# Optimization experiments

Measured on AMD Instinct MI355X. Metric: run time of the kernel, lower is better.

Reference implementation:

```python
import jax, jax.numpy as jnp
import numpy as np

B, IH, IW = 16, 32, 32
N = IH * IW
HEADS, DIM_HEAD = 8, 64
INNER = HEADS * DIM_HEAD  # 512
INP, OUP = 512, 512
SCALE = DIM_HEAD ** -0.5


def _relative_index():
    # replicate torch.meshgrid (ij) -> coords [2, N]
    yy, xx = np.meshgrid(np.arange(IH), np.arange(IW), indexing='ij')
    coords = np.stack([yy.reshape(-1), xx.reshape(-1)])  # [2, N]
    rel = coords[:, :, None] - coords[:, None, :]        # [2, N, N]
    rel[0] += IH - 1
    rel[1] += IW - 1
    rel[0] *= 2 * IW - 1
    return jnp.asarray(rel.sum(0).reshape(-1), dtype=jnp.int32)  # [N*N]


def setup_inputs() -> dict:
    key = jax.random.key(0)
    k1, k2, k3, k4, k5 = jax.random.split(key, 5)
    x = jax.random.normal(k1, (B, N, INP), dtype=jnp.float32)
    W_qkv = jax.random.normal(k2, (INP, 3 * INNER), dtype=jnp.float32) * (INP ** -0.5)
    # table is initialized to zeros in the module; use small randn so bias path is exercised
    rel_table = jax.random.normal(k3, ((2 * IH - 1) * (2 * IW - 1), HEADS), dtype=jnp.float32) * 0.02
    W_out = jax.random.normal(k4, (INNER, OUP), dtype=jnp.float32) * (INNER ** -0.5)
    b_out = jax.random.normal(k5, (OUP,), dtype=jnp.float32) * 0.02
    return {
        'x': x,
        'W_qkv': W_qkv,
        'rel_table': rel_table,
        'W_out': W_out,
        'b_out': b_out,
        'rel_index': _relative_index(),
    }


def reference(x, W_qkv, rel_table, W_out, b_out, rel_index):
    b, n, _ = x.shape
    qkv = x @ W_qkv                                            # [b, n, 3*inner]
    q, k, v = jnp.split(qkv, 3, axis=-1)
    def to_heads(t):
        return t.reshape(b, n, HEADS, DIM_HEAD).transpose(0, 2, 1, 3)  # [b, h, n, d]
    q, k, v = to_heads(q), to_heads(k), to_heads(v)
    dots = jnp.einsum('bhnd,bhmd->bhnm', q, k) * SCALE         # [b, h, n, n]
    bias = rel_table[rel_index].reshape(n, n, HEADS).transpose(2, 0, 1)[None]  # [1, h, n, n]
    attn = jax.nn.softmax(dots + bias, axis=-1)
    out = jnp.einsum('bhnm,bhmd->bhnd', attn, v)               # [b, h, n, d]
    out = out.transpose(0, 2, 1, 3).reshape(b, n, INNER)       # [b, n, inner]
    return out @ W_out + b_out
```

## Files before the change

kernel.cpp:

```cpp
#include <hip/hip_runtime.h>
#include <math.h>

#define BATCH 16
#define NTOK 1024
#define HEADS 8
#define DHEAD 64
#define INNER 512
#define QKV_COLS 1536
#define SCALE_L2E 0.1803368801111244f
#define LOG2E 1.4426950408889634f

#if __has_builtin(__builtin_amdgcn_exp2f)
#define EXP2F(x) __builtin_amdgcn_exp2f(x)
#else
#define EXP2F(x) __expf((x) * 0.6931471805599453f)
#endif

typedef _Float16 f16x8 __attribute__((ext_vector_type(8)));
typedef _Float16 f16x4 __attribute__((ext_vector_type(4)));
typedef float f32x4 __attribute__((ext_vector_type(4)));

#define MFMA32(a, b, c) __builtin_amdgcn_mfma_f32_16x16x32_f16(a, b, c, 0, 0, 0)

__device__ __forceinline__ void glds16(const void* g, void* l) {
    __builtin_amdgcn_global_load_lds(
        (const __attribute__((address_space(1))) unsigned int*)g,
        (__attribute__((address_space(3))) unsigned int*)l, 16, 0, 0);
}

#define XV (BATCH * NTOK * INNER / 4)
#define WQ (INNER * QKV_COLS)
#define WO (INNER * INNER)

__global__ __launch_bounds__(256)
void convert_inputs(const float* __restrict__ x, const float* __restrict__ Wq,
                    const float* __restrict__ Wo, _Float16* __restrict__ x_h,
                    _Float16* __restrict__ Wq_t, _Float16* __restrict__ Wo_t) {
    int idx = blockIdx.x * 256 + threadIdx.x;
    if (idx < XV) {
        float4 v = ((const float4*)x)[idx];
        f16x4 h;
        h[0] = (_Float16)v.x; h[1] = (_Float16)v.y;
        h[2] = (_Float16)v.z; h[3] = (_Float16)v.w;
        *(f16x4*)(x_h + (size_t)idx * 4) = h;
    } else if (idx < XV + WQ) {
        int i = idx - XV;
        int n = i >> 9, k = i & 511;
        Wq_t[i] = (_Float16)Wq[k * QKV_COLS + n];
    } else if (idx < XV + WQ + WO) {
        int i = idx - XV - WQ;
        int n = i >> 9, k = i & 511;
        Wo_t[i] = (_Float16)Wo[k * INNER + n];
    }
}

__global__ __launch_bounds__(256, 2)
void gemm_qkv(const _Float16* __restrict__ A, const _Float16* __restrict__ Bt,
              _Float16* __restrict__ qkv, _Float16* __restrict__ vtg,
              int M, int N, int K) {
    __shared__ _Float16 As[3][128 * 32];
    __shared__ _Float16 Bs[3][256 * 32];

    const int t    = threadIdx.x;
    const int l    = t & 63;
    const int w    = t >> 6;
    const int wm   = w >> 1;
    const int wn   = w & 1;
    const int quad = l >> 4;
    const int lrow = l & 15;

    const int nwg = gridDim.x * gridDim.y;
    int bid = blockIdx.x + gridDim.x * blockIdx.y;
    bid = (bid & 7) * (nwg >> 3) + (bid >> 3);
    const size_t row0 = (size_t)(bid / gridDim.x) * 128;
    const size_t col0 = (size_t)(bid % gridDim.x) * 256;

    const int srow = t >> 2;
    const int sch  = t & 3;

    f32x4 acc[4][8] = {};
    const int NSTEP = K >> 5;

    auto stage = [&](int kk, int bufi) {
#pragma unroll
        for (int p = 0; p < 2; ++p) {
            const int r  = p * 64 + srow;
            const int gc = (sch ^ ((r >> 1) & 3)) * 8;
            glds16(A + (row0 + r) * K + kk * 32 + gc,
                   (char*)As[bufi] + p * 4096 + t * 16);
        }
#pragma unroll
        for (int p = 0; p < 4; ++p) {
            const int r  = p * 64 + srow;
            const int gc = (sch ^ ((r >> 1) & 3)) * 8;
            glds16(Bt + (col0 + r) * K + kk * 32 + gc,
                   (char*)Bs[bufi] + p * 4096 + t * 16);
        }
    };

    stage(0, 0);
    stage(1, 1);

    int buf = 0, pre = 2;
    for (int kk = 0; kk < NSTEP; ++kk) {
        if (kk + 1 < NSTEP) asm volatile("s_waitcnt vmcnt(6)" ::: "memory");
        else                asm volatile("s_waitcnt vmcnt(0)" ::: "memory");
        __builtin_amdgcn_s_barrier();
        __builtin_amdgcn_sched_barrier(0);
        if (kk + 2 < NSTEP) stage(kk + 2, pre);

        f16x8 af[4], bf[8];
#pragma unroll
        for (int i = 0; i < 4; ++i) {
            const int r = wm * 64 + i * 16 + lrow;
            af[i] = *(const f16x8*)(As[buf] + r * 32 + ((quad ^ ((r >> 1) & 3)) * 8));
        }
#pragma unroll
        for (int j = 0; j < 4; ++j) {
            const int r = wn * 128 + j * 16 + lrow;
            bf[j] = *(const f16x8*)(Bs[buf] + r * 32 + ((quad ^ ((r >> 1) & 3)) * 8));
        }
#pragma unroll
        for (int i = 0; i < 4; ++i)
#pragma unroll
            for (int j = 0; j < 4; ++j)
                acc[i][j] = MFMA32(bf[j], af[i], acc[i][j]);
#pragma unroll
        for (int j = 4; j < 8; ++j) {
            const int r = wn * 128 + j * 16 + lrow;
            bf[j] = *(const f16x8*)(Bs[buf] + r * 32 + ((quad ^ ((r >> 1) & 3)) * 8));
        }
#pragma unroll
        for (int i = 0; i < 4; ++i)
#pragma unroll
            for (int j = 4; j < 8; ++j)
                acc[i][j] = MFMA32(bf[j], af[i], acc[i][j]);

        buf = (buf == 2) ? 0 : buf + 1;
        pre = (pre == 2) ? 0 : pre + 1;
    }

    const bool isV = (col0 >= 2 * INNER);
#pragma unroll
    for (int i = 0; i < 4; ++i) {
        const size_t m = row0 + wm * 64 + i * 16 + lrow;
#pragma unroll
        for (int j = 0; j < 8; ++j) {
            const size_t c = col0 + wn * 128 + j * 16 + quad * 4;
            f32x4 v = acc[i][j];
            if (!isV) {
                f16x4 hv;
                hv[0] = (_Float16)v[0]; hv[1] = (_Float16)v[1];
                hv[2] = (_Float16)v[2]; hv[3] = (_Float16)v[3];
                *(f16x4*)(qkv + m * N + c) = hv;
            } else {
                const int cv = (int)(c - 2 * INNER);
                const int hh = cv >> 6, db = cv & 63;
                const size_t vb = (((size_t)(m >> 10) * HEADS + hh) * 64 + db) * NTOK
                                  + (m & (NTOK - 1));
#pragma unroll
                for (int reg = 0; reg < 4; ++reg)
                    vtg[vb + (size_t)reg * NTOK] = (_Float16)v[reg];
            }
        }
    }
}

__global__ __launch_bounds__(256, 3)
void gemm_out(const _Float16* __restrict__ A, const _Float16* __restrict__ Bt,
              const float* __restrict__ bias, float* __restrict__ Cout,
              int M, int N, int K) {
    __shared__ _Float16 As[3][128 * 32];
    __shared__ _Float16 Bs[3][128 * 32];

    const int t    = threadIdx.x;
    const int l    = t & 63;
    const int w    = t >> 6;
    const int wm   = w >> 1;
    const int wn   = w & 1;
    const int quad = l >> 4;
    const int lrow = l & 15;

    const int nwg = gridDim.x * gridDim.y;
    int bid = blockIdx.x + gridDim.x * blockIdx.y;
    bid = (bid & 7) * (nwg >> 3) + (bid >> 3);
    const size_t row0 = (size_t)(bid / gridDim.x) * 128;
    const size_t col0 = (size_t)(bid % gridDim.x) * 128;

    const int srow = t >> 2;
    const int sch  = t & 3;

    f32x4 acc[4][4] = {};
    const int NSTEP = K >> 5;

    auto stage = [&](int kk, int bufi) {
#pragma unroll
        for (int p = 0; p < 2; ++p) {
            const int r  = p * 64 + srow;
            const int gc = (sch ^ ((r >> 1) & 3)) * 8;
            glds16(A  + (row0 + r) * K + kk * 32 + gc, (char*)As[bufi] + p * 4096 + t * 16);
            glds16(Bt + (col0 + r) * K + kk * 32 + gc, (char*)Bs[bufi] + p * 4096 + t * 16);
        }
    };

    stage(0, 0);
    stage(1, 1);

    int buf = 0, pre = 2;
    for (int kk = 0; kk < NSTEP; ++kk) {
        if (kk + 1 < NSTEP) asm volatile("s_waitcnt vmcnt(4)" ::: "memory");
        else                asm volatile("s_waitcnt vmcnt(0)" ::: "memory");
        __builtin_amdgcn_s_barrier();
        __builtin_amdgcn_sched_barrier(0);
        if (kk + 2 < NSTEP) stage(kk + 2, pre);

        f16x8 af[4], bf[4];
#pragma unroll
        for (int i = 0; i < 4; ++i) {
            const int r = wm * 64 + i * 16 + lrow;
            af[i] = *(const f16x8*)(As[buf] + r * 32 + ((quad ^ ((r >> 1) & 3)) * 8));
        }
#pragma unroll
        for (int j = 0; j < 4; ++j) {
            const int r = wn * 64 + j * 16 + lrow;
            bf[j] = *(const f16x8*)(Bs[buf] + r * 32 + ((quad ^ ((r >> 1) & 3)) * 8));
        }
#pragma unroll
        for (int i = 0; i < 4; ++i)
#pragma unroll
            for (int j = 0; j < 4; ++j)
                acc[i][j] = MFMA32(bf[j], af[i], acc[i][j]);

        buf = (buf == 2) ? 0 : buf + 1;
        pre = (pre == 2) ? 0 : pre + 1;
    }

#pragma unroll
    for (int i = 0; i < 4; ++i) {
        const size_t m = row0 + wm * 64 + i * 16 + lrow;
#pragma unroll
        for (int j = 0; j < 4; ++j) {
            const size_t c = col0 + wn * 64 + j * 16 + quad * 4;
            f32x4 v = acc[i][j];
            float4 bv = *(const float4*)(bias + c);
            v[0] += bv.x; v[1] += bv.y; v[2] += bv.z; v[3] += bv.w;
            *(f32x4*)(Cout + m * N + c) = v;
        }
    }
}

__global__ __launch_bounds__(512, 4)
void attn_f16_v7(const _Float16* __restrict__ qkv, const _Float16* __restrict__ vt,
                 const float* __restrict__ rel_table, _Float16* __restrict__ out) {
    __shared__ _Float16 Ks[2][64 * 64];
    __shared__ _Float16 Vs[2][64 * 64];
    __shared__ float biasS[3969];

    const int t    = threadIdx.x;
    const int l    = t & 63;
    const int w    = t >> 6;
    const int quad = l >> 4;
    const int lrow = l & 15;
    const int h    = blockIdx.y;
    const int bb   = blockIdx.z;
    const int qr0  = blockIdx.x * 256 + w * 32;

    for (int idx = t; idx < 3969; idx += 512)
        biasS[idx] = rel_table[idx * HEADS + h] * LOG2E;

    const size_t tokbase = (size_t)bb * NTOK;

    f16x8 aq[2][2];
#pragma unroll
    for (int mt = 0; mt < 2; ++mt)
#pragma unroll
        for (int ksi = 0; ksi < 2; ++ksi)
            aq[mt][ksi] = *(const f16x8*)(qkv + (tokbase + qr0 + mt * 16 + lrow) * QKV_COLS
                                          + h * DHEAD + ksi * 32 + quad * 8);

    f32x4 O[2][4] = {};
    float l0 = 0.f, l1 = 0.f;

    const int iy = qr0 >> 5;
    const int krow_base = 8 * (lrow >> 2) + (lrow & 3);
    const int fKl = (lrow & 3) + 4 * ((lrow >> 2) & 1);

    const int kr  = t >> 3;
    const int ksl = t & 7;
    const int fKr = (kr & 3) + 4 * ((kr >> 3) & 1);
    const _Float16* kbase = qkv + tokbase * QKV_COLS + INNER + h * DHEAD;
    const _Float16* vbase = vt + ((size_t)(bb * HEADS + h) * 64) * NTOK;

    auto stage = [&](int jt, int bufi) {
        const int j0s = jt * 64;
        glds16(kbase + (size_t)(j0s + kr) * QKV_COLS + (ksl ^ fKr) * 8, (char*)Ks[bufi] + t * 16);
        glds16(vbase + (size_t)kr * NTOK + j0s + (ksl ^ (kr & 7)) * 8,  (char*)Vs[bufi] + t * 16);
    };

    stage(0, 0);

    for (int jt = 0; jt < 16; ++jt) {
        const int buf = jt & 1;
        __syncthreads();
        if (jt < 15) stage(jt + 1, buf ^ 1);

#pragma unroll
        for (int jn0 = 0; jn0 < 2; ++jn0) {
            f16x8 pb0, pb1;
#pragma unroll
            for (int s = 0; s < 2; ++s) {
                const int krow = jn0 * 32 + krow_base + 4 * s;
                f32x4 S0 = {}, S1 = {};
                __builtin_amdgcn_s_setprio(1);
#pragma unroll
                for (int ksi = 0; ksi < 2; ++ksi) {
                    f16x8 bk = *(const f16x8*)(Ks[buf] + krow * 64
                                               + (((ksi * 4 + quad) ^ fKl) * 8));
                    S0 = MFMA32(bk, aq[0][ksi], S0);
                    S1 = MFMA32(bk, aq[1][ksi], S1);
                }
                __builtin_amdgcn_s_setprio(0);
                const int base = (iy - (jt * 2 + jn0) + 31) * 63 + 31 + lrow
                                 - 8 * quad - 4 * s;
                {
                    float p0 = EXP2F(fmaf(S0[0], SCALE_L2E, biasS[base - 0]));
                    float p1 = EXP2F(fmaf(S0[1], SCALE_L2E, biasS[base - 1]));
                    float p2 = EXP2F(fmaf(S0[2], SCALE_L2E, biasS[base - 2]));
                    float p3 = EXP2F(fmaf(S0[3], SCALE_L2E, biasS[base - 3]));
                    l0 += (p0 + p1) + (p2 + p3);
                    pb0[s * 4 + 0] = (_Float16)p0; pb0[s * 4 + 1] = (_Float16)p1;
                    pb0[s * 4 + 2] = (_Float16)p2; pb0[s * 4 + 3] = (_Float16)p3;
                }
                {
                    const int b1 = base + 16;
                    float p0 = EXP2F(fmaf(S1[0], SCALE_L2E, biasS[b1 - 0]));
                    float p1 = EXP2F(fmaf(S1[1], SCALE_L2E, biasS[b1 - 1]));
                    float p2 = EXP2F(fmaf(S1[2], SCALE_L2E, biasS[b1 - 2]));
                    float p3 = EXP2F(fmaf(S1[3], SCALE_L2E, biasS[b1 - 3]));
                    l1 += (p0 + p1) + (p2 + p3);
                    pb1[s * 4 + 0] = (_Float16)p0; pb1[s * 4 + 1] = (_Float16)p1;
                    pb1[s * 4 + 2] = (_Float16)p2; pb1[s * 4 + 3] = (_Float16)p3;
                }
            }

            __builtin_amdgcn_s_setprio(1);
#pragma unroll
            for (int dn = 0; dn < 4; ++dn) {
                const int d = dn * 16 + lrow;
                f16x8 av = *(const f16x8*)(Vs[buf] + d * 64
                              + (((jn0 * 4 + quad) ^ (d & 7)) * 8));
                O[0][dn] = MFMA32(av, pb0, O[0][dn]);
                O[1][dn] = MFMA32(av, pb1, O[1][dn]);
            }
            __builtin_amdgcn_s_setprio(0);
        }
    }

#pragma unroll
    for (int mt = 0; mt < 2; ++mt) {
        float s = mt ? l1 : l0;
        s += __shfl_xor(s, 16);
        s += __shfl_xor(s, 32);
        const float inv = 1.f / s;
        const size_t orow = (tokbase + qr0 + mt * 16 + lrow) * INNER + h * DHEAD;
#pragma unroll
        for (int dn = 0; dn < 4; ++dn) {
            const f32x4 o = O[mt][dn];
            f16x4 ov;
            ov[0] = (_Float16)(o[0] * inv); ov[1] = (_Float16)(o[1] * inv);
            ov[2] = (_Float16)(o[2] * inv); ov[3] = (_Float16)(o[3] * inv);
            *(f16x4*)(out + orow + dn * 16 + quad * 4) = ov;
        }
    }
}

extern "C" void kernel_launch(void* const* d_in, const int* in_sizes, int n_in,
                              void* d_out, int out_size, void* d_ws, size_t ws_size,
                              hipStream_t stream) {
    const float* x         = (const float*)d_in[0];
    const float* W_qkv     = (const float*)d_in[1];
    const float* rel_table = (const float*)d_in[2];
    const float* W_out     = (const float*)d_in[3];
    const float* b_out     = (const float*)d_in[4];

    _Float16* x_h   = (_Float16*)d_ws;
    _Float16* Wq_t  = x_h + (size_t)BATCH * NTOK * INNER;
    _Float16* Wo_t  = Wq_t + (size_t)INNER * QKV_COLS;
    _Float16* qkv_h = Wo_t + (size_t)INNER * INNER;
    _Float16* att_h = qkv_h + (size_t)BATCH * NTOK * QKV_COLS;
    _Float16* vt_g  = att_h + (size_t)BATCH * NTOK * INNER;

    const int M = BATCH * NTOK;

    convert_inputs<<<(XV + WQ + WO + 255) / 256, 256, 0, stream>>>(
        x, W_qkv, W_out, x_h, Wq_t, Wo_t);

    gemm_qkv<<<dim3(QKV_COLS / 256, M / 128), 256, 0, stream>>>(
        x_h, Wq_t, qkv_h, vt_g, M, QKV_COLS, INNER);

    attn_f16_v7<<<dim3(NTOK / 256, HEADS, BATCH), 512, 0, stream>>>(
        qkv_h, vt_g, rel_table, att_h);

    gemm_out<<<dim3(INNER / 128, M / 128), 256, 0, stream>>>(
        att_h, Wo_t, b_out, (float*)d_out, M, INNER, INNER);
}
```

Before: 207.4 us.

## Tile weight transpose-convert and shrink GEMM tiles for more workgroups

The weight conversion now reads 4x4 float blocks with vector loads and writes transposed f16x4 vectors, replacing the scalar strided gather with one element per thread. The QKV GEMM tile shrinks from 128x256 to 128x128 and the output GEMM from 128x128 to 128x64, which doubles the grid sizes and raises the occupancy hints. This is meant to fill more compute units and cut the cost of the strided transpose, at the price of less operand reuse per tile and more redundant A-tile loads.

```diff
diff --git a/kernel.cpp b/kernel.cpp
--- a/kernel.cpp
+++ b/kernel.cpp
@@ -29,37 +29,51 @@
 }
 
 #define XV (BATCH * NTOK * INNER / 4)
-#define WQ (INNER * QKV_COLS)
-#define WO (INNER * INNER)
+#define XB (XV / 256)
+#define WQTILES 192
+#define WOTILES 64
 
 __global__ __launch_bounds__(256)
 void convert_inputs(const float* __restrict__ x, const float* __restrict__ Wq,
                     const float* __restrict__ Wo, _Float16* __restrict__ x_h,
                     _Float16* __restrict__ Wq_t, _Float16* __restrict__ Wo_t) {
-    int idx = blockIdx.x * 256 + threadIdx.x;
-    if (idx < XV) {
+    const int b = blockIdx.x, t = threadIdx.x;
+    if (b < XB) {
+        const int idx = b * 256 + t;
         float4 v = ((const float4*)x)[idx];
         f16x4 h;
         h[0] = (_Float16)v.x; h[1] = (_Float16)v.y;
         h[2] = (_Float16)v.z; h[3] = (_Float16)v.w;
         *(f16x4*)(x_h + (size_t)idx * 4) = h;
-    } else if (idx < XV + WQ) {
-        int i = idx - XV;
-        int n = i >> 9, k = i & 511;
-        Wq_t[i] = (_Float16)Wq[k * QKV_COLS + n];
-    } else if (idx < XV + WQ + WO) {
-        int i = idx - XV - WQ;
-        int n = i >> 9, k = i & 511;
-        Wo_t[i] = (_Float16)Wo[k * INNER + n];
-    }
-}
-
-__global__ __launch_bounds__(256, 2)
+        return;
+    }
+    const bool isQ = (b < XB + WQTILES);
+    const int b2  = isQ ? (b - XB) : (b - XB - WQTILES);
+    const int ntl = isQ ? 24 : 8;
+    const int ldw = isQ ? QKV_COLS : INNER;
+    const float*   W  = isQ ? Wq   : Wo;
+    _Float16*      Wt = isQ ? Wq_t : Wo_t;
+    const int k0 = (b2 / ntl) * 64, n0 = (b2 % ntl) * 64;
+    const int kk = k0 + (t >> 4) * 4, nn = n0 + (t & 15) * 4;
+    f32x4 v0 = *(const f32x4*)(W + (size_t)(kk + 0) * ldw + nn);
+    f32x4 v1 = *(const f32x4*)(W + (size_t)(kk + 1) * ldw + nn);
+    f32x4 v2 = *(const f32x4*)(W + (size_t)(kk + 2) * ldw + nn);
+    f32x4 v3 = *(const f32x4*)(W + (size_t)(kk + 3) * ldw + nn);
+#pragma unroll
+    for (int f = 0; f < 4; ++f) {
+        f16x4 h;
+        h[0] = (_Float16)v0[f]; h[1] = (_Float16)v1[f];
+        h[2] = (_Float16)v2[f]; h[3] = (_Float16)v3[f];
+        *(f16x4*)(Wt + (size_t)(nn + f) * INNER + kk) = h;
+    }
+}
+
+__global__ __launch_bounds__(256, 3)
 void gemm_qkv(const _Float16* __restrict__ A, const _Float16* __restrict__ Bt,
               _Float16* __restrict__ qkv, _Float16* __restrict__ vtg,
               int M, int N, int K) {
     __shared__ _Float16 As[3][128 * 32];
-    __shared__ _Float16 Bs[3][256 * 32];
+    __shared__ _Float16 Bs[3][128 * 32];
 
     const int t    = threadIdx.x;
     const int l    = t & 63;
@@ -73,12 +87,12 @@
     int bid = blockIdx.x + gridDim.x * blockIdx.y;
     bid = (bid & 7) * (nwg >> 3) + (bid >> 3);
     const size_t row0 = (size_t)(bid / gridDim.x) * 128;
-    const size_t col0 = (size_t)(bid % gridDim.x) * 256;
+    const size_t col0 = (size_t)(bid % gridDim.x) * 128;
 
     const int srow = t >> 2;
     const int sch  = t & 3;
 
-    f32x4 acc[4][8] = {};
+    f32x4 acc[4][4] = {};
     const int NSTEP = K >> 5;
 
     auto stage = [&](int kk, int bufi) {
@@ -86,15 +100,8 @@
         for (int p = 0; p < 2; ++p) {
             const int r  = p * 64 + srow;
             const int gc = (sch ^ ((r >> 1) & 3)) * 8;
-            glds16(A + (row0 + r) * K + kk * 32 + gc,
-                   (char*)As[bufi] + p * 4096 + t * 16);
-        }
-#pragma unroll
-        for (int p = 0; p < 4; ++p) {
-            const int r  = p * 64 + srow;
-            const int gc = (sch ^ ((r >> 1) & 3)) * 8;
-            glds16(Bt + (col0 + r) * K + kk * 32 + gc,
-                   (char*)Bs[bufi] + p * 4096 + t * 16);
+            glds16(A  + (row0 + r) * K + kk * 32 + gc, (char*)As[bufi] + p * 4096 + t * 16);
+            glds16(Bt + (col0 + r) * K + kk * 32 + gc, (char*)Bs[bufi] + p * 4096 + t * 16);
         }
     };
 
@@ -103,13 +110,13 @@
 
     int buf = 0, pre = 2;
     for (int kk = 0; kk < NSTEP; ++kk) {
-        if (kk + 1 < NSTEP) asm volatile("s_waitcnt vmcnt(6)" ::: "memory");
+        if (kk + 1 < NSTEP) asm volatile("s_waitcnt vmcnt(4)" ::: "memory");
         else                asm volatile("s_waitcnt vmcnt(0)" ::: "memory");
         __builtin_amdgcn_s_barrier();
         __builtin_amdgcn_sched_barrier(0);
         if (kk + 2 < NSTEP) stage(kk + 2, pre);
 
-        f16x8 af[4], bf[8];
+        f16x8 af[4], bf[4];
 #pragma unroll
         for (int i = 0; i < 4; ++i) {
             const int r = wm * 64 + i * 16 + lrow;
@@ -117,7 +124,7 @@
         }
 #pragma unroll
         for (int j = 0; j < 4; ++j) {
-            const int r = wn * 128 + j * 16 + lrow;
+            const int r = wn * 64 + j * 16 + lrow;
             bf[j] = *(const f16x8*)(Bs[buf] + r * 32 + ((quad ^ ((r >> 1) & 3)) * 8));
         }
 #pragma unroll
@@ -125,16 +132,6 @@
 #pragma unroll
             for (int j = 0; j < 4; ++j)
                 acc[i][j] = MFMA32(bf[j], af[i], acc[i][j]);
-#pragma unroll
-        for (int j = 4; j < 8; ++j) {
-            const int r = wn * 128 + j * 16 + lrow;
-            bf[j] = *(const f16x8*)(Bs[buf] + r * 32 + ((quad ^ ((r >> 1) & 3)) * 8));
-        }
-#pragma unroll
-        for (int i = 0; i < 4; ++i)
-#pragma unroll
-            for (int j = 4; j < 8; ++j)
-                acc[i][j] = MFMA32(bf[j], af[i], acc[i][j]);
 
         buf = (buf == 2) ? 0 : buf + 1;
         pre = (pre == 2) ? 0 : pre + 1;
@@ -145,8 +142,8 @@
     for (int i = 0; i < 4; ++i) {
         const size_t m = row0 + wm * 64 + i * 16 + lrow;
 #pragma unroll
-        for (int j = 0; j < 8; ++j) {
-            const size_t c = col0 + wn * 128 + j * 16 + quad * 4;
+        for (int j = 0; j < 4; ++j) {
+            const size_t c = col0 + wn * 64 + j * 16 + quad * 4;
             f32x4 v = acc[i][j];
             if (!isV) {
                 f16x4 hv;
@@ -166,12 +163,12 @@
     }
 }
 
-__global__ __launch_bounds__(256, 3)
+__global__ __launch_bounds__(256, 4)
 void gemm_out(const _Float16* __restrict__ A, const _Float16* __restrict__ Bt,
               const float* __restrict__ bias, float* __restrict__ Cout,
               int M, int N, int K) {
     __shared__ _Float16 As[3][128 * 32];
-    __shared__ _Float16 Bs[3][128 * 32];
+    __shared__ _Float16 Bs[3][64 * 32];
 
     const int t    = threadIdx.x;
     const int l    = t & 63;
@@ -185,12 +182,12 @@
     int bid = blockIdx.x + gridDim.x * blockIdx.y;
     bid = (bid & 7) * (nwg >> 3) + (bid >> 3);
     const size_t row0 = (size_t)(bid / gridDim.x) * 128;
-    const size_t col0 = (size_t)(bid % gridDim.x) * 128;
+    const size_t col0 = (size_t)(bid % gridDim.x) * 64;
 
     const int srow = t >> 2;
     const int sch  = t & 3;
 
-    f32x4 acc[4][4] = {};
+    f32x4 acc[4][2] = {};
     const int NSTEP = K >> 5;
 
     auto stage = [&](int kk, int bufi) {
@@ -198,8 +195,14 @@
         for (int p = 0; p < 2; ++p) {
             const int r  = p * 64 + srow;
             const int gc = (sch ^ ((r >> 1) & 3)) * 8;
-            glds16(A  + (row0 + r) * K + kk * 32 + gc, (char*)As[bufi] + p * 4096 + t * 16);
-            glds16(Bt + (col0 + r) * K + kk * 32 + gc, (char*)Bs[bufi] + p * 4096 + t * 16);
+            glds16(A + (row0 + r) * K + kk * 32 + gc,
+                   (char*)As[bufi] + p * 4096 + t * 16);
+        }
+        {
+            const int r  = srow;
+            const int gc = (sch ^ ((r >> 1) & 3)) * 8;
+            glds16(Bt + (col0 + r) * K + kk * 32 + gc,
+                   (char*)Bs[bufi] + t * 16);
         }
     };
 
@@ -208,27 +211,27 @@
 
     int buf = 0, pre = 2;
     for (int kk = 0; kk < NSTEP; ++kk) {
-        if (kk + 1 < NSTEP) asm volatile("s_waitcnt vmcnt(4)" ::: "memory");
+        if (kk + 1 < NSTEP) asm volatile("s_waitcnt vmcnt(3)" ::: "memory");
         else                asm volatile("s_waitcnt vmcnt(0)" ::: "memory");
         __builtin_amdgcn_s_barrier();
         __builtin_amdgcn_sched_barrier(0);
         if (kk + 2 < NSTEP) stage(kk + 2, pre);
 
-        f16x8 af[4], bf[4];
+        f16x8 af[4], bf[2];
 #pragma unroll
         for (int i = 0; i < 4; ++i) {
             const int r = wm * 64 + i * 16 + lrow;
             af[i] = *(const f16x8*)(As[buf] + r * 32 + ((quad ^ ((r >> 1) & 3)) * 8));
         }
 #pragma unroll
-        for (int j = 0; j < 4; ++j) {
-            const int r = wn * 64 + j * 16 + lrow;
+        for (int j = 0; j < 2; ++j) {
+            const int r = wn * 32 + j * 16 + lrow;
             bf[j] = *(const f16x8*)(Bs[buf] + r * 32 + ((quad ^ ((r >> 1) & 3)) * 8));
         }
 #pragma unroll
         for (int i = 0; i < 4; ++i)
 #pragma unroll
-            for (int j = 0; j < 4; ++j)
+            for (int j = 0; j < 2; ++j)
                 acc[i][j] = MFMA32(bf[j], af[i], acc[i][j]);
 
         buf = (buf == 2) ? 0 : buf + 1;
@@ -239,8 +242,8 @@
     for (int i = 0; i < 4; ++i) {
         const size_t m = row0 + wm * 64 + i * 16 + lrow;
 #pragma unroll
-        for (int j = 0; j < 4; ++j) {
-            const size_t c = col0 + wn * 64 + j * 16 + quad * 4;
+        for (int j = 0; j < 2; ++j) {
+            const size_t c = col0 + wn * 32 + j * 16 + quad * 4;
             f32x4 v = acc[i][j];
             float4 bv = *(const float4*)(bias + c);
             v[0] += bv.x; v[1] += bv.y; v[2] += bv.z; v[3] += bv.w;
@@ -392,15 +395,15 @@
 
     const int M = BATCH * NTOK;
 
-    convert_inputs<<<(XV + WQ + WO + 255) / 256, 256, 0, stream>>>(
+    convert_inputs<<<XB + WQTILES + WOTILES, 256, 0, stream>>>(
         x, W_qkv, W_out, x_h, Wq_t, Wo_t);
 
-    gemm_qkv<<<dim3(QKV_COLS / 256, M / 128), 256, 0, stream>>>(
+    gemm_qkv<<<dim3(QKV_COLS / 128, M / 128), 256, 0, stream>>>(
         x_h, Wq_t, qkv_h, vt_g, M, QKV_COLS, INNER);
 
     attn_f16_v7<<<dim3(NTOK / 256, HEADS, BATCH), 512, 0, stream>>>(
         qkv_h, vt_g, rel_table, att_h);
 
-    gemm_out<<<dim3(INNER / 128, M / 128), 256, 0, stream>>>(
+    gemm_out<<<dim3(INNER / 64, M / 128), 256, 0, stream>>>(
         att_h, Wo_t, b_out, (float*)d_out, M, INNER, INNER);
 }
```

Result: slower. 215.1 us (+3.7%).
